# Kernel optimization log

Measured on AMD Instinct MI355X. Metric: run time of the kernel, lower is better.

The kernel has to match this reference:

```python
import jax, jax.numpy as jnp
import numpy as np

CODEBOOK_SIZE = 1024
EMB_DIM = 64


def setup_inputs() -> dict:
    key = jax.random.key(0)
    k1, k2 = jax.random.split(key)
    z = jax.random.normal(k1, (4, EMB_DIM, 32, 32, 32), dtype=jnp.float32)
    embedding = jax.random.normal(k2, (CODEBOOK_SIZE, EMB_DIM), dtype=jnp.float32)
    return {"z": z, "embedding": embedding}


def reference(z, embedding):
    # z: [b, c, h, w, d], embedding: [K, c]
    b, c, h, w, d = z.shape
    K = embedding.shape[0]
    # flatten to [N, c] with channels last (matches permute(0,2,3,4,1).reshape)
    zf = jnp.transpose(z, (0, 2, 3, 4, 1)).reshape(-1, c)
    # squared L2 distance to each codebook entry: ||z||^2 - 2 z.e + ||e||^2
    dist = (
        jnp.sum(zf * zf, axis=1, keepdims=True)
        - 2.0 * zf @ embedding.T
        + jnp.sum(embedding * embedding, axis=1)[None, :]
    )  # [N, K]
    min_encoding_indices = jnp.argmin(dist, axis=1)  # [N]
    # one-hot @ embedding == gather (same math, no NxK materialization)
    z_q = embedding[min_encoding_indices]  # [N, c]
    z_q = jnp.transpose(z_q.reshape(b, h, w, d, c), (0, 4, 1, 2, 3))
    # straight-through estimator
    z_q = z + jax.lax.stop_gradient(z_q - z)
    # perplexity from mean one-hot occupancy
    n_tokens = zf.shape[0]
    e_mean = jnp.bincount(min_encoding_indices, length=K).astype(zf.dtype) / n_tokens
    perplexity = jnp.exp(-jnp.sum(e_mean * jnp.log(e_mean + 1e-10)))
    loss = jnp.asarray(0.0, dtype=z.dtype)
    return (
        z_q,
        loss,
        perplexity,
        min_encoding_indices.reshape(b, h, w, d),
        jnp.mean(dist),
    )
```

## Files before the change

### kernel.cpp

```cpp
#include <hip/hip_runtime.h>

#define CH     64
#define KC     1024
#define SP     32768
#define NBATCH 4
#define NTOK   (NBATCH * SP)
#define MTOK   64
#define SZZ    68
#define ECH    128
#define NCHK   (KC / ECH)
#define SZEB   72
#define CAP    16
#define MARGIN 3.0f

#define OFF_ZQ   0
#define OFF_LOSS (NBATCH * CH * SP)
#define OFF_PERP (OFF_LOSS + 1)
#define OFF_IDX  (OFF_PERP + 1)
#define OFF_MEAN (OFF_IDX + NTOK)


typedef __attribute__((ext_vector_type(8))) short  s16x8;
typedef __attribute__((ext_vector_type(4))) float  f32x4;

__device__ __forceinline__ unsigned short f2bf(float f) {
    unsigned int u = __float_as_uint(f);
    return (unsigned short)((u + 0x7fffu + ((u >> 16) & 1u)) >> 16);
}

__device__ __forceinline__ float exact_dist(const float* zrow,
                                            const float* __restrict__ emb,
                                            const float* enl, int c) {
    const float4* er = (const float4*)(emb + (size_t)c * CH);
    float a0 = 0.f, a1 = 0.f, a2 = 0.f, a3 = 0.f;
#pragma unroll
    for (int j = 0; j < 16; ++j) {
        float4 e4 = er[j];
        a0 = fmaf(zrow[4 * j + 0], e4.x, a0);
        a1 = fmaf(zrow[4 * j + 1], e4.y, a1);
        a2 = fmaf(zrow[4 * j + 2], e4.z, a2);
        a3 = fmaf(zrow[4 * j + 3], e4.w, a3);
    }
    return enl[c] - 2.f * ((a0 + a1) + (a2 + a3));
}

__global__ __launch_bounds__(256) void prep(const float* __restrict__ e,
                                            int* __restrict__ hist,
                                            float* __restrict__ sums,
                                            float* __restrict__ sum_zc,
                                            float* __restrict__ sum_ec,
                                            float* __restrict__ enorm,
                                            unsigned short* __restrict__ eb) {
    const int tid = threadIdx.x;
    const int bk = blockIdx.x;
    if (bk < 4) {
        int k = bk * 256 + tid;
        const float4* row = (const float4*)(e + (size_t)k * CH);
        float n = 0.f;
#pragma unroll
        for (int j = 0; j < CH / 4; ++j) {
            float4 v = row[j];
            n += v.x * v.x + v.y * v.y + v.z * v.z + v.w * v.w;
        }
        enorm[k] = n;
    } else if (bk == 4) {
        if (tid == 0) sums[0] = 0.f;
        if (tid < 64) sum_zc[tid] = 0.f;
        __shared__ float ls1[256];
        __shared__ float r2[4];
        int c = tid & 63;
        int strip = tid >> 6;
        float s1 = 0.f, s2 = 0.f;
        for (int k = strip * 256; k < strip * 256 + 256; ++k) {
            float v = e[k * CH + c];
            s1 += v;
            s2 = fmaf(v, v, s2);
        }
        ls1[tid] = s1;
        for (int off = 32; off; off >>= 1) s2 += __shfl_down(s2, off);
        if ((tid & 63) == 0) r2[tid >> 6] = s2;
        __syncthreads();
        if (strip == 0) sum_ec[c] = ls1[c] + ls1[64 + c] + ls1[128 + c] + ls1[192 + c];
        if (tid == 0) sums[1] = r2[0] + r2[1] + r2[2] + r2[3];
    } else if (bk < 9) {
        hist[(bk - 5) * 256 + tid] = 0;
    } else {
        int base = (bk - 9) * 16384;
        for (int j = 0; j < 64; ++j) {
            int i = base + tid + j * 256;
            eb[i] = f2bf(e[i]);
        }
    }
}

__global__ __launch_bounds__(256, 2) void vq_main(const float* __restrict__ z,
                                                  const float* __restrict__ emb,
                                                  const unsigned short* __restrict__ eb,
                                                  const float* __restrict__ enorm,
                                                  float* __restrict__ out,
                                                  int* __restrict__ hist,
                                                  float* __restrict__ sums,
                                                  float* __restrict__ sum_zc) {
    __shared__ float zl[MTOK * SZZ];
    __shared__ unsigned short ebl[ECH * SZEB];
    __shared__ float enorm_l[KC];
    __shared__ float dmin_l[MTOK];
    __shared__ float zs1[256], zs2[256];
    __shared__ int   cand[MTOK][CAP];
    __shared__ int   ccnt[MTOK];
    __shared__ int   fi[MTOK];

    const int tid = threadIdx.x;
    const int w = tid >> 6;
    const int lane = tid & 63;
    const int n15 = lane & 15;
    const int q = lane >> 4;
    const int t0 = blockIdx.x * MTOK;
    const int bb = t0 >> 15;
    const int s0 = t0 & (SP - 1);

    {
        const float* zbase = z + ((size_t)bb * CH) * SP + s0;
#pragma unroll
        for (int j = 0; j < 4; ++j) {
            int idx = tid + j * 256;
            int c = idx >> 4;
            int tq = idx & 15;
            float4 v = *(const float4*)(zbase + (size_t)c * SP + tq * 4);
            zl[(4 * tq + 0) * SZZ + c] = v.x;
            zl[(4 * tq + 1) * SZZ + c] = v.y;
            zl[(4 * tq + 2) * SZZ + c] = v.z;
            zl[(4 * tq + 3) * SZZ + c] = v.w;
        }
#pragma unroll
        for (int j = 0; j < 4; ++j) enorm_l[tid + j * 256] = enorm[tid + j * 256];
        if (tid < MTOK) ccnt[tid] = 0;
    }
    __syncthreads();

    s16x8 A0, A1;
    {
        const float* zrow = &zl[(w * 16 + n15) * SZZ];
        float4 za = *(const float4*)(zrow + q * 8);
        float4 zb = *(const float4*)(zrow + q * 8 + 4);
        float4 zc = *(const float4*)(zrow + 32 + q * 8);
        float4 zd = *(const float4*)(zrow + 32 + q * 8 + 4);
        A0[0] = (short)f2bf(za.x); A0[1] = (short)f2bf(za.y);
        A0[2] = (short)f2bf(za.z); A0[3] = (short)f2bf(za.w);
        A0[4] = (short)f2bf(zb.x); A0[5] = (short)f2bf(zb.y);
        A0[6] = (short)f2bf(zb.z); A0[7] = (short)f2bf(zb.w);
        A1[0] = (short)f2bf(zc.x); A1[1] = (short)f2bf(zc.y);
        A1[2] = (short)f2bf(zc.z); A1[3] = (short)f2bf(zc.w);
        A1[4] = (short)f2bf(zd.x); A1[5] = (short)f2bf(zd.y);
        A1[6] = (short)f2bf(zd.z); A1[7] = (short)f2bf(zd.w);
    }
    const unsigned short* ebq = ebl + (size_t)n15 * SZEB + q * 8;

    float bmin[4] = {3.4e38f, 3.4e38f, 3.4e38f, 3.4e38f};
    for (int ch = 0; ch < NCHK; ++ch) {
        __syncthreads();
#pragma unroll
        for (int rep = 0; rep < ECH * 8 / 256; ++rep) {
            int i = tid + rep * 256;
            int row = i >> 3, j = i & 7;
            ((float4*)&ebl[row * SZEB])[j] =
                ((const float4*)(eb + (size_t)(ch * ECH + row) * CH))[j];
        }
        __syncthreads();
        for (int ct = 0; ct < ECH / 16; ++ct) {
            const unsigned short* p = ebq + ct * 16 * SZEB;
            s16x8 B0 = *(const s16x8*)p;
            s16x8 B1 = *(const s16x8*)(p + 32);
            f32x4 acc = {0.f, 0.f, 0.f, 0.f};
            acc = __builtin_amdgcn_mfma_f32_16x16x32_bf16(A0, B0, acc, 0, 0, 0);
            acc = __builtin_amdgcn_mfma_f32_16x16x32_bf16(A1, B1, acc, 0, 0, 0);
            float en = enorm_l[ch * ECH + ct * 16 + n15];
#pragma unroll
            for (int r = 0; r < 4; ++r) {
                float d = fmaf(-2.f, acc[r], en);
                bmin[r] = fminf(bmin[r], d);
            }
        }
    }
#pragma unroll
    for (int off = 1; off < 16; off <<= 1)
#pragma unroll
        for (int r = 0; r < 4; ++r)
            bmin[r] = fminf(bmin[r], __shfl_xor(bmin[r], off));
    if (n15 == 0)
#pragma unroll
        for (int r = 0; r < 4; ++r) dmin_l[w * 16 + 4 * q + r] = bmin[r];
    __syncthreads();

    float thr[4];
#pragma unroll
    for (int r = 0; r < 4; ++r) thr[r] = dmin_l[w * 16 + 4 * q + r] + MARGIN;
    for (int cc = 0; cc < NCHK; ++cc) {
        int ch = (cc == 0) ? (NCHK - 1) : (cc - 1);
        if (cc) {
            __syncthreads();
#pragma unroll
            for (int rep = 0; rep < ECH * 8 / 256; ++rep) {
                int i = tid + rep * 256;
                int row = i >> 3, j = i & 7;
                ((float4*)&ebl[row * SZEB])[j] =
                    ((const float4*)(eb + (size_t)(ch * ECH + row) * CH))[j];
            }
            __syncthreads();
        }
        for (int ct = 0; ct < ECH / 16; ++ct) {
            const unsigned short* p = ebq + ct * 16 * SZEB;
            s16x8 B0 = *(const s16x8*)p;
            s16x8 B1 = *(const s16x8*)(p + 32);
            f32x4 acc = {0.f, 0.f, 0.f, 0.f};
            acc = __builtin_amdgcn_mfma_f32_16x16x32_bf16(A0, B0, acc, 0, 0, 0);
            acc = __builtin_amdgcn_mfma_f32_16x16x32_bf16(A1, B1, acc, 0, 0, 0);
            float en = enorm_l[ch * ECH + ct * 16 + n15];
#pragma unroll
            for (int r = 0; r < 4; ++r) {
                float d = fmaf(-2.f, acc[r], en);
                if (d <= thr[r]) {
                    int t = w * 16 + 4 * q + r;
                    int pos = atomicAdd(&ccnt[t], 1);
                    if (pos < CAP) cand[t][pos] = ch * ECH + ct * 16 + n15;
                }
            }
        }
    }
    __syncthreads();

    if (tid < MTOK) {
        int t = tid;
        const float* zrow = &zl[t * SZZ];
        int cnt = ccnt[t];
        float best = 3.4e38f;
        int bi = 0;
        if (cnt <= CAP) {
            for (int j = 0; j < cnt; ++j) {
                int c = cand[t][j];
                float d = exact_dist(zrow, emb, enorm_l, c);
                if (d < best || (d == best && c < bi)) { best = d; bi = c; }
            }
        } else {
            for (int c = 0; c < KC; ++c) {
                float d = exact_dist(zrow, emb, enorm_l, c);
                if (d < best) { best = d; bi = c; }
            }
        }
        fi[t] = bi;
        out[OFF_IDX + t0 + t] = (float)bi;
        atomicAdd(&hist[bi], 1);
    }
    __syncthreads();

#pragma unroll
    for (int j = 0; j < 16; ++j) {
        int idx = tid + j * 256;
        int c = idx >> 6;
        int t = idx & 63;
        int code = fi[t];
        float ev = emb[(size_t)code * CH + c];
        float zv = zl[t * SZZ + c];
        out[OFF_ZQ + ((size_t)bb * CH + c) * SP + s0 + t] = zv + (ev - zv);
    }

    {
        int c = tid >> 2, qq = tid & 3;
        float s1 = 0.f, s2 = 0.f;
        for (int tt = 0; tt < 16; ++tt) {
            float v = zl[(qq * 16 + tt) * SZZ + c];
            s1 += v;
            s2 = fmaf(v, v, s2);
        }
        zs1[tid] = s1;
        zs2[tid] = s2;
    }
    __syncthreads();
    if (tid < 64) {
        float a = zs1[4 * tid] + zs1[4 * tid + 1] + zs1[4 * tid + 2] + zs1[4 * tid + 3];
        atomicAdd(&sum_zc[tid], a);
        float bsum = zs2[4 * tid] + zs2[4 * tid + 1] + zs2[4 * tid + 2] + zs2[4 * tid + 3];
        for (int off = 32; off; off >>= 1) bsum += __shfl_down(bsum, off);
        if (tid == 0) atomicAdd(&sums[0], bsum);
    }
}

__global__ __launch_bounds__(1024) void finalize(const int* __restrict__ hist,
                                                 const float* __restrict__ sums,
                                                 const float* __restrict__ sum_zc,
                                                 const float* __restrict__ sum_ec,
                                                 float* __restrict__ out) {
    __shared__ float red[1024];
    int k = threadIdx.x;
    float p = (float)hist[k] * (1.0f / (float)NTOK);
    red[k] = p * logf(p + 1e-10f);
    __syncthreads();
    for (int off = 512; off; off >>= 1) {
        if (k < off) red[k] += red[k + off];
        __syncthreads();
    }
    if (k == 0) {
        out[OFF_PERP] = expf(-red[0]);
        out[OFF_LOSS] = 0.f;
        double dot = 0.0;
        for (int c = 0; c < CH; ++c) dot += (double)sum_zc[c] * (double)sum_ec[c];
        double mean = ((double)KC * (double)sums[0] + (double)NTOK * (double)sums[1] - 2.0 * dot)
                      / ((double)NTOK * (double)KC);
        out[OFF_MEAN] = (float)mean;
    }
}

extern "C" void kernel_launch(void* const* d_in, const int* in_sizes, int n_in,
                              void* d_out, int out_size, void* d_ws, size_t ws_size,
                              hipStream_t stream) {
    const float* z   = (const float*)d_in[0];
    const float* emb = (const float*)d_in[1];
    float* out = (float*)d_out;

    int*            hist   = (int*)d_ws;
    float*          sums   = (float*)d_ws + 1024;
    float*          sum_zc = (float*)d_ws + 1026;
    float*          sum_ec = (float*)d_ws + 1090;
    float*          enorm  = (float*)d_ws + 1154;
    unsigned short* eb     = (unsigned short*)((int*)d_ws + 4096);

    prep<<<13, 256, 0, stream>>>(emb, hist, sums, sum_zc, sum_ec, enorm, eb);
    vq_main<<<NTOK / MTOK, 256, 0, stream>>>(z, emb, eb, enorm, out, hist, sums, sum_zc);
    finalize<<<1, 1024, 0, stream>>>(hist, sums, sum_zc, sum_ec, out);
}
```

Baseline: 217.4 us.

## Track per-lane top-two distances to drop second MFMA candidate pass

Each lane now tracks its best and second-best approximate distance and the best code during the first MFMA sweep. This removes the second full pass over the codebook (reloading all chunks and redoing the MFMAs) that collected candidates within a margin. Lanes whose second-best also falls within the margin are marked dirty, and their whole strided column (64 codes) is rescored exactly in the fallback loop. The change adds compare and select work to the hot loop and leaves a serial exact rescoring cost, run by one thread per token, whenever near-ties are common.

```diff
diff --git a/kernel.cpp b/kernel.cpp
--- a/kernel.cpp
+++ b/kernel.cpp
@@ -108,6 +108,7 @@
     __shared__ float zs1[256], zs2[256];
     __shared__ int   cand[MTOK][CAP];
     __shared__ int   ccnt[MTOK];
+    __shared__ int   dirty[MTOK];
     __shared__ int   fi[MTOK];
 
     const int tid = threadIdx.x;
@@ -134,7 +135,7 @@
         }
 #pragma unroll
         for (int j = 0; j < 4; ++j) enorm_l[tid + j * 256] = enorm[tid + j * 256];
-        if (tid < MTOK) ccnt[tid] = 0;
+        if (tid < MTOK) { ccnt[tid] = 0; dirty[tid] = 0; }
     }
     __syncthreads();
 
@@ -156,7 +157,9 @@
     }
     const unsigned short* ebq = ebl + (size_t)n15 * SZEB + q * 8;
 
-    float bmin[4] = {3.4e38f, 3.4e38f, 3.4e38f, 3.4e38f};
+    float min1[4] = {3.4e38f, 3.4e38f, 3.4e38f, 3.4e38f};
+    float min2[4] = {3.4e38f, 3.4e38f, 3.4e38f, 3.4e38f};
+    int   c1[4]   = {0, 0, 0, 0};
     for (int ch = 0; ch < NCHK; ++ch) {
         __syncthreads();
 #pragma unroll
@@ -175,13 +178,23 @@
             acc = __builtin_amdgcn_mfma_f32_16x16x32_bf16(A0, B0, acc, 0, 0, 0);
             acc = __builtin_amdgcn_mfma_f32_16x16x32_bf16(A1, B1, acc, 0, 0, 0);
             float en = enorm_l[ch * ECH + ct * 16 + n15];
+            int code = ch * ECH + ct * 16 + n15;
 #pragma unroll
             for (int r = 0; r < 4; ++r) {
                 float d = fmaf(-2.f, acc[r], en);
-                bmin[r] = fminf(bmin[r], d);
-            }
-        }
-    }
+                if (d < min1[r]) {
+                    min2[r] = min1[r];
+                    min1[r] = d;
+                    c1[r] = code;
+                } else if (d < min2[r]) {
+                    min2[r] = d;
+                }
+            }
+        }
+    }
+    float bmin[4];
+#pragma unroll
+    for (int r = 0; r < 4; ++r) bmin[r] = min1[r];
 #pragma unroll
     for (int off = 1; off < 16; off <<= 1)
 #pragma unroll
@@ -192,39 +205,18 @@
         for (int r = 0; r < 4; ++r) dmin_l[w * 16 + 4 * q + r] = bmin[r];
     __syncthreads();
 
-    float thr[4];
-#pragma unroll
-    for (int r = 0; r < 4; ++r) thr[r] = dmin_l[w * 16 + 4 * q + r] + MARGIN;
-    for (int cc = 0; cc < NCHK; ++cc) {
-        int ch = (cc == 0) ? (NCHK - 1) : (cc - 1);
-        if (cc) {
-            __syncthreads();
-#pragma unroll
-            for (int rep = 0; rep < ECH * 8 / 256; ++rep) {
-                int i = tid + rep * 256;
-                int row = i >> 3, j = i & 7;
-                ((float4*)&ebl[row * SZEB])[j] =
-                    ((const float4*)(eb + (size_t)(ch * ECH + row) * CH))[j];
-            }
-            __syncthreads();
-        }
-        for (int ct = 0; ct < ECH / 16; ++ct) {
-            const unsigned short* p = ebq + ct * 16 * SZEB;
-            s16x8 B0 = *(const s16x8*)p;
-            s16x8 B1 = *(const s16x8*)(p + 32);
-            f32x4 acc = {0.f, 0.f, 0.f, 0.f};
-            acc = __builtin_amdgcn_mfma_f32_16x16x32_bf16(A0, B0, acc, 0, 0, 0);
-            acc = __builtin_amdgcn_mfma_f32_16x16x32_bf16(A1, B1, acc, 0, 0, 0);
-            float en = enorm_l[ch * ECH + ct * 16 + n15];
-#pragma unroll
-            for (int r = 0; r < 4; ++r) {
-                float d = fmaf(-2.f, acc[r], en);
-                if (d <= thr[r]) {
-                    int t = w * 16 + 4 * q + r;
-                    int pos = atomicAdd(&ccnt[t], 1);
-                    if (pos < CAP) cand[t][pos] = ch * ECH + ct * 16 + n15;
-                }
-            }
+    {
+        float thr[4];
+#pragma unroll
+        for (int r = 0; r < 4; ++r) thr[r] = dmin_l[w * 16 + 4 * q + r] + MARGIN;
+#pragma unroll
+        for (int r = 0; r < 4; ++r) {
+            int t = w * 16 + 4 * q + r;
+            if (min1[r] <= thr[r]) {
+                int pos = atomicAdd(&ccnt[t], 1);
+                if (pos < CAP) cand[t][pos] = c1[r];
+            }
+            if (min2[r] <= thr[r]) atomicOr(&dirty[t], 1 << n15);
         }
     }
     __syncthreads();
@@ -247,6 +239,15 @@
                 if (d < best) { best = d; bi = c; }
             }
         }
+        int dm = dirty[t];
+        while (dm) {
+            int ln = __ffs((unsigned)dm) - 1;
+            dm &= dm - 1;
+            for (int c = ln; c < KC; c += 16) {
+                float d = exact_dist(zrow, emb, enorm_l, c);
+                if (d < best || (d == best && c < bi)) { best = d; bi = c; }
+            }
+        }
         fi[t] = bi;
         out[OFF_IDX + t0 + t] = (float)bi;
         atomicAdd(&hist[bi], 1);
```

New measurement: 346.2 us. +59.3%, slower.
